# Performance work log

Measured on AMD Instinct MI355X. Metric: run time of the kernel, lower is better.

## Reference

```python
import jax, jax.numpy as jnp
import numpy as np

N = 4096
IN_FEATS = 64
HIDDEN = 128
STEPS = 3
SCALE = 3.0
LJ_EPS = 0.1
LJ_SIGMA = 3.5
LJ_MIX = 0.1  # 'auto' branch: pot = exp(-r/scale)*relu(score) + 0.1*lj
LN_EPS = 1e-5


def setup_inputs() -> dict:
    key = jax.random.key(0)
    ks = jax.random.split(key, 12)
    x = jax.random.normal(ks[0], (N, IN_FEATS), dtype=jnp.float32)
    # sparse-ish 0/1 adjacency (float, as multiplied in the torch code)
    adj = (jax.random.uniform(ks[1], (N, N)) < 0.02).astype(jnp.float32)
    # positive pairwise distances in Angstrom-like range
    dist_mat = jax.random.uniform(ks[2], (N, N), dtype=jnp.float32) * 10.0 + 0.5
    s_in = 1.0 / np.sqrt(IN_FEATS)
    s_h = 1.0 / np.sqrt(HIDDEN)
    s_2h = 1.0 / np.sqrt(2 * HIDDEN)
    params = {
        'W_in': jax.random.uniform(ks[3], (IN_FEATS, HIDDEN), minval=-s_in, maxval=s_in),
        'b_in': jnp.zeros((HIDDEN,), jnp.float32),
        'W_msg': jax.random.uniform(ks[4], (HIDDEN, HIDDEN), minval=-s_h, maxval=s_h),
        'b_msg': jnp.zeros((HIDDEN,), jnp.float32),
        'W_u1': jax.random.uniform(ks[5], (2 * HIDDEN, HIDDEN), minval=-s_2h, maxval=s_2h),
        'b_u1': jnp.zeros((HIDDEN,), jnp.float32),
        'W_u2': jax.random.uniform(ks[6], (HIDDEN, HIDDEN), minval=-s_h, maxval=s_h),
        'b_u2': jnp.zeros((HIDDEN,), jnp.float32),
        'gamma': jnp.ones((HIDDEN,), jnp.float32),
        'beta': jnp.zeros((HIDDEN,), jnp.float32),
    }
    return {'x': x, 'adj': adj, 'dist_mat': dist_mat, **params}


def _layernorm(x, gamma, beta):
    mu = jnp.mean(x, axis=-1, keepdims=True)
    var = jnp.mean(jnp.square(x - mu), axis=-1, keepdims=True)
    return (x - mu) * jax.lax.rsqrt(var + LN_EPS) * gamma + beta


def reference(x, adj, dist_mat, W_in, b_in, W_msg, b_msg, W_u1, b_u1, W_u2, b_u2, gamma, beta):
    h = x @ W_in + b_in  # (n, hidden)
    # distance-only terms are loop-invariant
    r_safe = jnp.clip(dist_mat, 1e-6, None)
    sr6 = (LJ_SIGMA / r_safe) ** 6
    lj = 4.0 * LJ_EPS * (sr6 * sr6 - sr6)          # (n, n)
    decay = jnp.exp(-dist_mat / SCALE)             # (n, n)
    pot_const = LJ_MIX * lj                        # 'auto' branch constant part
    for _ in range(STEPS):
        # torch code computes msg_lin(h) but never uses it (dead code) -> skipped
        # pot_scalar[i,j] = <h_i, h_j>, computed without (n,n,d) materialization
        pot_scalar = h @ h.T                       # (n, n)
        pot = decay * jax.nn.relu(pot_scalar) + pot_const
        # m_i = sum_j pot[i,j]*adj[i,j]*h_j == masked-weighted matmul
        m = (pot * adj) @ h                        # (n, hidden)
        concat = jnp.concatenate([h, m], axis=-1)  # (n, 2*hidden)
        delta = jax.nn.relu(concat @ W_u1 + b_u1) @ W_u2 + b_u2
        h = _layernorm(h + delta, gamma, beta)
    return h
```

## Files before the change

kernel.cpp:

```cpp
#include <hip/hip_runtime.h>
#include <hip/hip_bf16.h>

#define NN   4096
#define HID  128
#define INFE 64
#define KE   160
#define KMAX 192
#define CH   64
#define RPB  4
#define RPB8 8

typedef unsigned short u16;
typedef unsigned int   u32;

__device__ __forceinline__ float bfu(u16 u) { return __uint_as_float(((u32)u) << 16); }
__device__ __forceinline__ float bflo(u32 w){ return __uint_as_float(w << 16); }
__device__ __forceinline__ float bfhi(u32 w){ return __uint_as_float(w & 0xffff0000u); }
__device__ __forceinline__ u16 f2b(float f) { __hip_bfloat16 h = __float2bfloat16(f); return *(u16*)&h; }

template<int CTRL>
__device__ __forceinline__ float dppadd(float v) {
    return v + __uint_as_float((u32)__builtin_amdgcn_update_dpp(
        0, (int)__float_as_uint(v), CTRL, 0xF, 0xF, true));
}

__global__ __launch_bounds__(128) void k_h0(
    const float* __restrict__ x, const float* __restrict__ Win, const float* __restrict__ bin,
    float* __restrict__ hdst, u16* __restrict__ bdst)
{
    __shared__ float xl[INFE];
    const int r = blockIdx.x;
    const int d = threadIdx.x;
    if (d < INFE) xl[d] = x[(size_t)r*INFE + d];
    __syncthreads();
    float acc = bin[d];
    #pragma unroll 8
    for (int k = 0; k < INFE; ++k)
        acc = fmaf(xl[k], Win[k*HID + d], acc);
    hdst[(size_t)r*HID + d] = acc;
    bdst[(size_t)r*HID + d] = f2b(acc);
}

__global__ __launch_bounds__(256) void k_prep(
    const float* __restrict__ adj, const float* __restrict__ dist,
    float4* __restrict__ edges, int* __restrict__ nnzp,
    const float* __restrict__ x, const float* __restrict__ Win, const float* __restrict__ bin,
    float* __restrict__ hdst, u16* __restrict__ bdst)
{
    const int t = threadIdx.x;
    if (blockIdx.x < NN/2) {
        __shared__ int cnt[2];
        __shared__ int   cl[2][KE];
        __shared__ float ca[2][KE];
        const int r0 = blockIdx.x * 2;
        if (t < 2) cnt[t] = 0;
        __syncthreads();
        float4 av[2][4];
        #pragma unroll
        for (int rr = 0; rr < 2; ++rr) {
            const float4* arow = (const float4*)(adj + (size_t)(r0+rr)*NN);
            #pragma unroll
            for (int q = 0; q < 4; ++q) av[rr][q] = arow[t + 256*q];
        }
        #pragma unroll
        for (int rr = 0; rr < 2; ++rr) {
            #pragma unroll
            for (int q = 0; q < 4; ++q) {
                float a4[4] = {av[rr][q].x, av[rr][q].y, av[rr][q].z, av[rr][q].w};
                if (a4[0] != 0.f || a4[1] != 0.f || a4[2] != 0.f || a4[3] != 0.f) {
                    #pragma unroll
                    for (int u = 0; u < 4; ++u) {
                        if (a4[u] != 0.f) {
                            int pos = atomicAdd(&cnt[rr], 1);
                            if (pos < KE) { cl[rr][pos] = 4*(t + 256*q) + u; ca[rr][pos] = a4[u]; }
                        }
                    }
                }
            }
        }
        __syncthreads();
        #pragma unroll
        for (int rr = 0; rr < 2; ++rr) {
            const int n  = cnt[rr] < KE ? cnt[rr] : KE;
            const int np = (n + 31) / 32 * 32;
            float4* erow = edges + (size_t)(r0+rr)*KE;
            for (int i = n + t; i < np; i += 256)
                erow[i] = make_float4(__int_as_float(0), 0.f, 0.f, 0.f);
            const float* drow = dist + (size_t)(r0+rr)*NN;
            for (int i = t; i < n; i += 256) {
                int   c = cl[rr][i];
                float a = ca[rr][i];
                float d  = fmaxf(drow[c], 1e-6f);
                float dw1 = a * __expf(-d * (1.0f/3.0f));
                float tt = 3.5f / d, t2 = tt*tt, t6 = t2*t2*t2;
                float dw2 = a * 0.04f * (t6*t6 - t6);
                erow[i] = make_float4(__int_as_float(c), dw1, dw2, 0.f);
            }
            if (t == 0) nnzp[r0+rr] = np;
        }
    } else {
        __shared__ float xl[2][INFE];
        const int grp = t >> 7;
        const int d   = t & 127;
        const int r   = (blockIdx.x - NN/2) * 2 + grp;
        if (d < INFE) xl[grp][d] = x[(size_t)r*INFE + d];
        __syncthreads();
        float acc = bin[d];
        #pragma unroll 8
        for (int k = 0; k < INFE; ++k)
            acc = fmaf(xl[grp][k], Win[k*HID + d], acc);
        hdst[(size_t)r*HID + d] = acc;
        bdst[(size_t)r*HID + d] = f2b(acc);
    }
}

__global__ __launch_bounds__(512, 4) void k_fstep8(
    const float4* __restrict__ edges, const int* __restrict__ nnzp,
    const float* __restrict__ h, const u16* __restrict__ hb,
    const float* __restrict__ Wu1, const float* __restrict__ bu1,
    const float* __restrict__ Wu2, const float* __restrict__ bu2,
    const float* __restrict__ gam, const float* __restrict__ bet,
    float* __restrict__ hout, u16* __restrict__ bout)
{
    __shared__ __align__(16) float ps[8][RPB8][HID];
    __shared__ __align__(16) float hs[RPB8][HID];
    __shared__ __align__(16) float ms[RPB8][HID];
    __shared__ __align__(16) float h1s[RPB8][HID];
    __shared__ float hn[RPB8][HID];
    const int t    = threadIdx.x;
    const int w    = t >> 6;
    const int lane = t & 63;
    const int ig   = lane & 15;
    const int grp  = lane >> 4;
    const int r0   = blockIdx.x * RPB8;
    const int r    = r0 + w;

    const int np = nnzp[r];
    const float4 hiA = *(const float4*)(h + (size_t)r*HID + 8*ig);
    const float4 hiB = *(const float4*)(h + (size_t)r*HID + 8*ig + 4);
    if (grp == 0) {
        *(float4*)&hs[w][8*ig]     = hiA;
        *(float4*)&hs[w][8*ig + 4] = hiB;
    }

    const float4* erow = edges + (size_t)r*KE;
    float macc[8];
    #pragma unroll
    for (int d = 0; d < 8; ++d) macc[d] = 0.f;
    for (int e0 = 0; e0 < np; e0 += 32) {
        float4 ed[8]; uint4 hj4[8]; float p[8];
        #pragma unroll
        for (int q = 0; q < 8; ++q) ed[q] = erow[e0 + grp + 4*q];
        #pragma unroll
        for (int q = 0; q < 8; ++q) {
            int c = __float_as_int(ed[q].x);
            hj4[q] = *(const uint4*)(hb + (size_t)c*HID + 8*ig);
        }
        #pragma unroll
        for (int q = 0; q < 8; ++q) {
            float j0 = bflo(hj4[q].x), j1 = bfhi(hj4[q].x);
            float j2 = bflo(hj4[q].y), j3 = bfhi(hj4[q].y);
            float j4 = bflo(hj4[q].z), j5 = bfhi(hj4[q].z);
            float j6 = bflo(hj4[q].w), j7 = bfhi(hj4[q].w);
            float pp = hiA.x*j0;
            pp = fmaf(hiA.y, j1, pp); pp = fmaf(hiA.z, j2, pp); pp = fmaf(hiA.w, j3, pp);
            pp = fmaf(hiB.x, j4, pp); pp = fmaf(hiB.y, j5, pp); pp = fmaf(hiB.z, j6, pp);
            p[q] = fmaf(hiB.w, j7, pp);
        }
        #pragma unroll
        for (int q = 0; q < 8; ++q) {
            p[q] = dppadd<0x128>(p[q]);
            p[q] = dppadd<0x124>(p[q]);
            p[q] = dppadd<0x122>(p[q]);
            p[q] = dppadd<0x121>(p[q]);
        }
        #pragma unroll
        for (int q = 0; q < 8; ++q) {
            float wq = fmaf(ed[q].y, fmaxf(p[q], 0.f), ed[q].z);
            float j0 = bflo(hj4[q].x), j1 = bfhi(hj4[q].x);
            float j2 = bflo(hj4[q].y), j3 = bfhi(hj4[q].y);
            float j4 = bflo(hj4[q].z), j5 = bfhi(hj4[q].z);
            float j6 = bflo(hj4[q].w), j7 = bfhi(hj4[q].w);
            macc[0] = fmaf(wq, j0, macc[0]); macc[1] = fmaf(wq, j1, macc[1]);
            macc[2] = fmaf(wq, j2, macc[2]); macc[3] = fmaf(wq, j3, macc[3]);
            macc[4] = fmaf(wq, j4, macc[4]); macc[5] = fmaf(wq, j5, macc[5]);
            macc[6] = fmaf(wq, j6, macc[6]); macc[7] = fmaf(wq, j7, macc[7]);
        }
    }
    #pragma unroll
    for (int d = 0; d < 8; ++d) {
        macc[d] += __shfl_xor(macc[d], 16);
        macc[d] += __shfl_xor(macc[d], 32);
    }
    if (grp == 0) {
        *(float4*)&ms[w][8*ig]     = make_float4(macc[0], macc[1], macc[2], macc[3]);
        *(float4*)&ms[w][8*ig + 4] = make_float4(macc[4], macc[5], macc[6], macc[7]);
    }
    __syncthreads();

    {
        const int kq = t >> 6;
        const int dd = t & 63;
        const float bi0 = (kq == 0) ? bu1[dd]      : 0.f;
        const float bi1 = (kq == 0) ? bu1[dd + 64] : 0.f;
        float a0[RPB8], a1[RPB8];
        #pragma unroll
        for (int rr = 0; rr < RPB8; ++rr) { a0[rr] = bi0; a1[rr] = bi1; }
        const float (*src)[HID] = (kq < 4) ? hs : ms;
        const int kb = (kq & 3) * 32;
        const float* wp = Wu1 + (size_t)(kq * 32) * HID + dd;
        #pragma unroll 2
        for (int k = 0; k < 32; k += 4) {
            float w00 = wp[(k+0)*HID], w01 = wp[(k+0)*HID + 64];
            float w10 = wp[(k+1)*HID], w11 = wp[(k+1)*HID + 64];
            float w20 = wp[(k+2)*HID], w21 = wp[(k+2)*HID + 64];
            float w30 = wp[(k+3)*HID], w31 = wp[(k+3)*HID + 64];
            #pragma unroll
            for (int rr = 0; rr < RPB8; ++rr) {
                float4 c4 = *(const float4*)&src[rr][kb + k];
                a0[rr] = fmaf(c4.x, w00, a0[rr]); a0[rr] = fmaf(c4.y, w10, a0[rr]);
                a0[rr] = fmaf(c4.z, w20, a0[rr]); a0[rr] = fmaf(c4.w, w30, a0[rr]);
                a1[rr] = fmaf(c4.x, w01, a1[rr]); a1[rr] = fmaf(c4.y, w11, a1[rr]);
                a1[rr] = fmaf(c4.z, w21, a1[rr]); a1[rr] = fmaf(c4.w, w31, a1[rr]);
            }
        }
        #pragma unroll
        for (int rr = 0; rr < RPB8; ++rr) {
            ps[kq][rr][dd]      = a0[rr];
            ps[kq][rr][dd + 64] = a1[rr];
        }
    }
    __syncthreads();
    for (int pidx = t; pidx < RPB8*HID; pidx += 512) {
        int rr = pidx >> 7, d = pidx & 127;
        float s = ps[0][rr][d] + ps[1][rr][d] + ps[2][rr][d] + ps[3][rr][d]
                + ps[4][rr][d] + ps[5][rr][d] + ps[6][rr][d] + ps[7][rr][d];
        h1s[rr][d] = fmaxf(s, 0.f);
    }
    __syncthreads();
    {
        const int kq = t >> 6;
        const int dd = t & 63;
        const float bi0 = (kq == 0) ? bu2[dd]      : 0.f;
        const float bi1 = (kq == 0) ? bu2[dd + 64] : 0.f;
        float a0[RPB8], a1[RPB8];
        #pragma unroll
        for (int rr = 0; rr < RPB8; ++rr) { a0[rr] = bi0; a1[rr] = bi1; }
        const int kb = kq * 16;
        const float* wp = Wu2 + (size_t)(kq * 16) * HID + dd;
        #pragma unroll
        for (int k = 0; k < 16; k += 4) {
            float w00 = wp[(k+0)*HID], w01 = wp[(k+0)*HID + 64];
            float w10 = wp[(k+1)*HID], w11 = wp[(k+1)*HID + 64];
            float w20 = wp[(k+2)*HID], w21 = wp[(k+2)*HID + 64];
            float w30 = wp[(k+3)*HID], w31 = wp[(k+3)*HID + 64];
            #pragma unroll
            for (int rr = 0; rr < RPB8; ++rr) {
                float4 c4 = *(const float4*)&h1s[rr][kb + k];
                a0[rr] = fmaf(c4.x, w00, a0[rr]); a0[rr] = fmaf(c4.y, w10, a0[rr]);
                a0[rr] = fmaf(c4.z, w20, a0[rr]); a0[rr] = fmaf(c4.w, w30, a0[rr]);
                a1[rr] = fmaf(c4.x, w01, a1[rr]); a1[rr] = fmaf(c4.y, w11, a1[rr]);
                a1[rr] = fmaf(c4.z, w21, a1[rr]); a1[rr] = fmaf(c4.w, w31, a1[rr]);
            }
        }
        #pragma unroll
        for (int rr = 0; rr < RPB8; ++rr) {
            ps[kq][rr][dd]      = a0[rr];
            ps[kq][rr][dd + 64] = a1[rr];
        }
    }
    __syncthreads();
    for (int pidx = t; pidx < RPB8*HID; pidx += 512) {
        int rr = pidx >> 7, d = pidx & 127;
        hn[rr][d] = hs[rr][d]
                  + ps[0][rr][d] + ps[1][rr][d] + ps[2][rr][d] + ps[3][rr][d]
                  + ps[4][rr][d] + ps[5][rr][d] + ps[6][rr][d] + ps[7][rr][d];
    }
    __syncthreads();
    {
        float v0 = hn[w][lane], v1 = hn[w][lane + 64];
        float s = v0 + v1;
        #pragma unroll
        for (int mask = 1; mask <= 32; mask <<= 1) s += __shfl_xor(s, mask);
        float mu = s * (1.0f/128.0f);
        float z0 = v0 - mu, z1 = v1 - mu;
        float vv = fmaf(z0, z0, z1*z1);
        #pragma unroll
        for (int mask = 1; mask <= 32; mask <<= 1) vv += __shfl_xor(vv, mask);
        float rstd = rsqrtf(vv * (1.0f/128.0f) + 1e-5f);
        float o0 = fmaf(z0 * rstd, gam[lane],      bet[lane]);
        float o1 = fmaf(z1 * rstd, gam[lane + 64], bet[lane + 64]);
        hout[(size_t)r*HID + lane]      = o0;
        hout[(size_t)r*HID + lane + 64] = o1;
        bout[(size_t)r*HID + lane]      = f2b(o0);
        bout[(size_t)r*HID + lane + 64] = f2b(o1);
    }
}

template<bool SB, bool DB>
__global__ __launch_bounds__(128) void k_step(
    const float* __restrict__ adj, const float* __restrict__ dist,
    const void* hsrc, void* hdst,
    const float* __restrict__ Wu1, const float* __restrict__ bu1,
    const float* __restrict__ Wu2, const float* __restrict__ bu2,
    const float* __restrict__ gam, const float* __restrict__ bet)
{
    __shared__ int   cnt4[RPB];
    __shared__ int   cl[RPB][KMAX];
    __shared__ float w1l[RPB][KMAX], w2l[RPB][KMAX];
    __shared__ __align__(16) float hs4[RPB][HID];
    __shared__ __align__(16) float hj[CH][HID + 1];
    __shared__ float pl[CH];
    __shared__ __align__(16) float ms[RPB][HID];
    __shared__ __align__(16) float h1s[RPB][HID];
    __shared__ float hn[RPB][HID];
    const int r0 = blockIdx.x * RPB;
    const int t  = threadIdx.x;
    const u16*   s16 = (const u16*)hsrc;
    const float* s32 = (const float*)hsrc;
    if (t < RPB) cnt4[t] = 0;
    for (int i = t; i < RPB*HID; i += 128) {
        int rr = i >> 7, d = i & 127;
        hs4[rr][d] = SB ? bfu(s16[(size_t)(r0+rr)*HID + d]) : s32[(size_t)(r0+rr)*HID + d];
    }
    __syncthreads();
    for (int idx = t; idx < RPB*(NN/4); idx += 128) {
        int rr = idx >> 10, c4 = idx & 1023;
        float4 a4 = ((const float4*)(adj + (size_t)(r0+rr)*NN))[c4];
        if (a4.x != 0.f || a4.y != 0.f || a4.z != 0.f || a4.w != 0.f) {
            const float* drow = dist + (size_t)(r0+rr)*NN;
            float av4[4] = {a4.x, a4.y, a4.z, a4.w};
            #pragma unroll
            for (int q = 0; q < 4; ++q) {
                float av = av4[q];
                if (av != 0.f) {
                    int c = 4*c4 + q;
                    float d  = fmaxf(drow[c], 1e-6f);
                    float dw1 = av * __expf(-d * (1.0f/3.0f));
                    float tt = 3.5f / d, t2 = tt*tt, t6 = t2*t2*t2;
                    float dw2 = av * 0.04f * (t6*t6 - t6);
                    int pos = atomicAdd(&cnt4[rr], 1);
                    if (pos < KMAX) { cl[rr][pos] = c; w1l[rr][pos] = dw1; w2l[rr][pos] = dw2; }
                }
            }
        }
    }
    __syncthreads();
    int npv[RPB];
    for (int rr = 0; rr < RPB; ++rr) {
        int n  = cnt4[rr] < KMAX ? cnt4[rr] : KMAX;
        int np = (n + CH - 1) / CH * CH;
        npv[rr] = np;
        for (int i = n + t; i < np; i += 128) { cl[rr][i] = 0; w1l[rr][i] = 0.f; w2l[rr][i] = 0.f; }
    }
    __syncthreads();
    const int e2 = t >> 1, hf = t & 1;
    for (int rr = 0; rr < RPB; ++rr) {
        float acc = 0.f;
        for (int e0 = 0; e0 < npv[rr]; e0 += CH) {
            int c = cl[rr][e0 + e2];
            float* dst = &hj[e2][hf*64];
            if (SB) {
                const uint4* sv = (const uint4*)(s16 + (size_t)c*HID + hf*64);
                #pragma unroll
                for (int i = 0; i < 8; ++i) {
                    uint4 v = sv[i];
                    dst[8*i+0] = __uint_as_float(v.x << 16); dst[8*i+1] = __uint_as_float(v.x & 0xffff0000u);
                    dst[8*i+2] = __uint_as_float(v.y << 16); dst[8*i+3] = __uint_as_float(v.y & 0xffff0000u);
                    dst[8*i+4] = __uint_as_float(v.z << 16); dst[8*i+5] = __uint_as_float(v.z & 0xffff0000u);
                    dst[8*i+6] = __uint_as_float(v.w << 16); dst[8*i+7] = __uint_as_float(v.w & 0xffff0000u);
                }
            } else {
                const float4* sv = (const float4*)(s32 + (size_t)c*HID + hf*64);
                #pragma unroll
                for (int i = 0; i < 16; ++i) {
                    float4 v = sv[i];
                    dst[4*i+0] = v.x; dst[4*i+1] = v.y; dst[4*i+2] = v.z; dst[4*i+3] = v.w;
                }
            }
            __syncthreads();
            {
                const float* ha = &hs4[rr][hf*64];
                const float* hb = &hj[e2][hf*64];
                float p = 0.f;
                #pragma unroll
                for (int i = 0; i < 64; ++i) p = fmaf(ha[i], hb[i], p);
                p += __shfl_xor(p, 1);
                if (hf == 0) pl[e2] = fmaf(w1l[rr][e0+e2], fmaxf(p, 0.f), w2l[rr][e0+e2]);
            }
            __syncthreads();
            #pragma unroll
            for (int i = 0; i < CH; ++i) acc = fmaf(pl[i], hj[i][t], acc);
            __syncthreads();
        }
        ms[rr][t] = acc;
    }
    __syncthreads();
    {
        float bb = bu1[t];
        float a0 = bb, a1 = bb, a2 = bb, a3 = bb;
        for (int k = 0; k < HID; k += 4) {
            float w0 = Wu1[(k+0)*HID + t], w1 = Wu1[(k+1)*HID + t];
            float w2 = Wu1[(k+2)*HID + t], w3 = Wu1[(k+3)*HID + t];
            float4 c0 = *(const float4*)&hs4[0][k];
            float4 c1 = *(const float4*)&hs4[1][k];
            float4 c2 = *(const float4*)&hs4[2][k];
            float4 c3 = *(const float4*)&hs4[3][k];
            a0 = fmaf(c0.x,w0,a0); a0 = fmaf(c0.y,w1,a0); a0 = fmaf(c0.z,w2,a0); a0 = fmaf(c0.w,w3,a0);
            a1 = fmaf(c1.x,w0,a1); a1 = fmaf(c1.y,w1,a1); a1 = fmaf(c1.z,w2,a1); a1 = fmaf(c1.w,w3,a1);
            a2 = fmaf(c2.x,w0,a2); a2 = fmaf(c2.y,w1,a2); a2 = fmaf(c2.z,w2,a2); a2 = fmaf(c2.w,w3,a2);
            a3 = fmaf(c3.x,w0,a3); a3 = fmaf(c3.y,w1,a3); a3 = fmaf(c3.z,w2,a3); a3 = fmaf(c3.w,w3,a3);
        }
        for (int k = 0; k < HID; k += 4) {
            float w0 = Wu1[(HID+k+0)*HID + t], w1 = Wu1[(HID+k+1)*HID + t];
            float w2 = Wu1[(HID+k+2)*HID + t], w3 = Wu1[(HID+k+3)*HID + t];
            float4 c0 = *(const float4*)&ms[0][k];
            float4 c1 = *(const float4*)&ms[1][k];
            float4 c2 = *(const float4*)&ms[2][k];
            float4 c3 = *(const float4*)&ms[3][k];
            a0 = fmaf(c0.x,w0,a0); a0 = fmaf(c0.y,w1,a0); a0 = fmaf(c0.z,w2,a0); a0 = fmaf(c0.w,w3,a0);
            a1 = fmaf(c1.x,w0,a1); a1 = fmaf(c1.y,w1,a1); a1 = fmaf(c1.z,w2,a1); a1 = fmaf(c1.w,w3,a1);
            a2 = fmaf(c2.x,w0,a2); a2 = fmaf(c2.y,w1,a2); a2 = fmaf(c2.z,w2,a2); a2 = fmaf(c2.w,w3,a2);
            a3 = fmaf(c3.x,w0,a3); a3 = fmaf(c3.y,w1,a3); a3 = fmaf(c3.z,w2,a3); a3 = fmaf(c3.w,w3,a3);
        }
        h1s[0][t] = fmaxf(a0,0.f); h1s[1][t] = fmaxf(a1,0.f);
        h1s[2][t] = fmaxf(a2,0.f); h1s[3][t] = fmaxf(a3,0.f);
    }
    __syncthreads();
    {
        float bb = bu2[t];
        float b0 = bb, b1 = bb, b2 = bb, b3 = bb;
        for (int k = 0; k < HID; k += 4) {
            float w0 = Wu2[(k+0)*HID + t], w1 = Wu2[(k+1)*HID + t];
            float w2 = Wu2[(k+2)*HID + t], w3 = Wu2[(k+3)*HID + t];
            float4 c0 = *(const float4*)&h1s[0][k];
            float4 c1 = *(const float4*)&h1s[1][k];
            float4 c2 = *(const float4*)&h1s[2][k];
            float4 c3 = *(const float4*)&h1s[3][k];
            b0 = fmaf(c0.x,w0,b0); b0 = fmaf(c0.y,w1,b0); b0 = fmaf(c0.z,w2,b0); b0 = fmaf(c0.w,w3,b0);
            b1 = fmaf(c1.x,w0,b1); b1 = fmaf(c1.y,w1,b1); b1 = fmaf(c1.z,w2,b1); b1 = fmaf(c1.w,w3,b1);
            b2 = fmaf(c2.x,w0,b2); b2 = fmaf(c2.y,w1,b2); b2 = fmaf(c2.z,w2,b2); b2 = fmaf(c2.w,w3,b2);
            b3 = fmaf(c3.x,w0,b3); b3 = fmaf(c3.y,w1,b3); b3 = fmaf(c3.z,w2,b3); b3 = fmaf(c3.w,w3,b3);
        }
        hn[0][t] = hs4[0][t] + b0; hn[1][t] = hs4[1][t] + b1;
        hn[2][t] = hs4[2][t] + b2; hn[3][t] = hs4[3][t] + b3;
    }
    __syncthreads();
    {
        const int lr = t >> 5, j = t & 31;
        float s = 0.f;
        #pragma unroll
        for (int q = 0; q < 4; ++q) s += hn[lr][j + 32*q];
        #pragma unroll
        for (int k2 = 16; k2 >= 1; k2 >>= 1) s += __shfl_xor(s, k2);
        float mu = s * (1.0f/128.0f);
        float v = 0.f;
        #pragma unroll
        for (int q = 0; q < 4; ++q) { float z = hn[lr][j + 32*q] - mu; v = fmaf(z, z, v); }
        #pragma unroll
        for (int k2 = 16; k2 >= 1; k2 >>= 1) v += __shfl_xor(v, k2);
        float rstd = rsqrtf(v * (1.0f/128.0f) + 1e-5f);
        #pragma unroll
        for (int q = 0; q < 4; ++q) {
            int dd = j + 32*q;
            float val = fmaf((hn[lr][dd] - mu) * rstd, gam[dd], bet[dd]);
            if (DB) ((u16*)hdst)[(size_t)(r0+lr)*HID + dd] = f2b(val);
            else    ((float*)hdst)[(size_t)(r0+lr)*HID + dd] = val;
        }
    }
}

extern "C" void kernel_launch(void* const* d_in, const int* in_sizes, int n_in,
                              void* d_out, int out_size, void* d_ws, size_t ws_size,
                              hipStream_t stream)
{
    const float* x    = (const float*)d_in[0];
    const float* adj  = (const float*)d_in[1];
    const float* dist = (const float*)d_in[2];
    const float* Win  = (const float*)d_in[3];
    const float* bin  = (const float*)d_in[4];
    const float* Wu1  = (const float*)d_in[7];
    const float* bu1  = (const float*)d_in[8];
    const float* Wu2  = (const float*)d_in[9];
    const float* bu2  = (const float*)d_in[10];
    const float* gam  = (const float*)d_in[11];
    const float* bet  = (const float*)d_in[12];

    const size_t ebytes = (size_t)NN * KE * sizeof(float4);
    const size_t cbytes = ((size_t)NN * sizeof(int) + 255) & ~255;
    const size_t hb32   = (size_t)NN * HID * sizeof(float);
    const size_t hb16   = (size_t)NN * HID * sizeof(u16);
    const size_t need   = ebytes + cbytes + hb32 + 2*hb16;

    if (ws_size >= need) {
        char* p = (char*)d_ws;
        float4* edges = (float4*)p;            p += ebytes;
        int*    nnzp  = (int*)p;               p += cbytes;
        float*  hA    = (float*)p;             p += hb32;
        u16*    bA    = (u16*)p;               p += hb16;
        u16*    bB    = (u16*)p;               p += hb16;
        float*  hB    = (float*)d_out;

        k_prep<<<NN/2 + NN/2, 256, 0, stream>>>(adj, dist, edges, nnzp, x, Win, bin, hA, bA);
        k_fstep8<<<NN/RPB8, 512, 0, stream>>>(edges, nnzp, hA, bA, Wu1, bu1, Wu2, bu2, gam, bet, hB, bB);
        k_fstep8<<<NN/RPB8, 512, 0, stream>>>(edges, nnzp, hB, bB, Wu1, bu1, Wu2, bu2, gam, bet, hA, bA);
        k_fstep8<<<NN/RPB8, 512, 0, stream>>>(edges, nnzp, hA, bA, Wu1, bu1, Wu2, bu2, gam, bet, hB, bB);
    } else if (ws_size >= hb32) {
        void* A = d_ws; void* B = d_out;
        k_h0<<<NN, 128, 0, stream>>>(x, Win, bin, (float*)A, (u16*)B);
        k_step<false,false><<<NN/RPB, 128, 0, stream>>>(adj, dist, A, B, Wu1, bu1, Wu2, bu2, gam, bet);
        k_step<false,false><<<NN/RPB, 128, 0, stream>>>(adj, dist, B, A, Wu1, bu1, Wu2, bu2, gam, bet);
        k_step<false,false><<<NN/RPB, 128, 0, stream>>>(adj, dist, A, B, Wu1, bu1, Wu2, bu2, gam, bet);
    }
}
```

Before: 224.8 us.

## Fuse prep and three GNN steps into one cooperative persistent kernel

Replaces the four separate launches (edge compaction plus input projection, then three step kernels) with a single cooperative kernel that uses grid-wide syncs between phases. Each block handles 8 rows for prep and reuses the shared-memory pool for the edge lists and the partial sums. The goal is to remove inter-kernel launch gaps and tail drain. It needs all 512 blocks of 512 threads to be co-resident; if the cooperative launch fails, it falls back to the old kernels. Grid syncs add their own barrier cost, and prep now runs fewer, larger blocks.

```diff
diff --git a/kernel.cpp b/kernel.cpp
--- a/kernel.cpp
+++ b/kernel.cpp
@@ -1,5 +1,8 @@
 #include <hip/hip_runtime.h>
 #include <hip/hip_bf16.h>
+#include <hip/hip_cooperative_groups.h>
+
+namespace cg = cooperative_groups;
 
 #define NN   4096
 #define HID  128
@@ -24,126 +27,24 @@
         0, (int)__float_as_uint(v), CTRL, 0xF, 0xF, true));
 }
 
-__global__ __launch_bounds__(128) void k_h0(
-    const float* __restrict__ x, const float* __restrict__ Win, const float* __restrict__ bin,
-    float* __restrict__ hdst, u16* __restrict__ bdst)
-{
-    __shared__ float xl[INFE];
-    const int r = blockIdx.x;
-    const int d = threadIdx.x;
-    if (d < INFE) xl[d] = x[(size_t)r*INFE + d];
-    __syncthreads();
-    float acc = bin[d];
-    #pragma unroll 8
-    for (int k = 0; k < INFE; ++k)
-        acc = fmaf(xl[k], Win[k*HID + d], acc);
-    hdst[(size_t)r*HID + d] = acc;
-    bdst[(size_t)r*HID + d] = f2b(acc);
-}
-
-__global__ __launch_bounds__(256) void k_prep(
-    const float* __restrict__ adj, const float* __restrict__ dist,
-    float4* __restrict__ edges, int* __restrict__ nnzp,
-    const float* __restrict__ x, const float* __restrict__ Win, const float* __restrict__ bin,
-    float* __restrict__ hdst, u16* __restrict__ bdst)
-{
-    const int t = threadIdx.x;
-    if (blockIdx.x < NN/2) {
-        __shared__ int cnt[2];
-        __shared__ int   cl[2][KE];
-        __shared__ float ca[2][KE];
-        const int r0 = blockIdx.x * 2;
-        if (t < 2) cnt[t] = 0;
-        __syncthreads();
-        float4 av[2][4];
-        #pragma unroll
-        for (int rr = 0; rr < 2; ++rr) {
-            const float4* arow = (const float4*)(adj + (size_t)(r0+rr)*NN);
-            #pragma unroll
-            for (int q = 0; q < 4; ++q) av[rr][q] = arow[t + 256*q];
-        }
-        #pragma unroll
-        for (int rr = 0; rr < 2; ++rr) {
-            #pragma unroll
-            for (int q = 0; q < 4; ++q) {
-                float a4[4] = {av[rr][q].x, av[rr][q].y, av[rr][q].z, av[rr][q].w};
-                if (a4[0] != 0.f || a4[1] != 0.f || a4[2] != 0.f || a4[3] != 0.f) {
-                    #pragma unroll
-                    for (int u = 0; u < 4; ++u) {
-                        if (a4[u] != 0.f) {
-                            int pos = atomicAdd(&cnt[rr], 1);
-                            if (pos < KE) { cl[rr][pos] = 4*(t + 256*q) + u; ca[rr][pos] = a4[u]; }
-                        }
-                    }
-                }
-            }
-        }
-        __syncthreads();
-        #pragma unroll
-        for (int rr = 0; rr < 2; ++rr) {
-            const int n  = cnt[rr] < KE ? cnt[rr] : KE;
-            const int np = (n + 31) / 32 * 32;
-            float4* erow = edges + (size_t)(r0+rr)*KE;
-            for (int i = n + t; i < np; i += 256)
-                erow[i] = make_float4(__int_as_float(0), 0.f, 0.f, 0.f);
-            const float* drow = dist + (size_t)(r0+rr)*NN;
-            for (int i = t; i < n; i += 256) {
-                int   c = cl[rr][i];
-                float a = ca[rr][i];
-                float d  = fmaxf(drow[c], 1e-6f);
-                float dw1 = a * __expf(-d * (1.0f/3.0f));
-                float tt = 3.5f / d, t2 = tt*tt, t6 = t2*t2*t2;
-                float dw2 = a * 0.04f * (t6*t6 - t6);
-                erow[i] = make_float4(__int_as_float(c), dw1, dw2, 0.f);
-            }
-            if (t == 0) nnzp[r0+rr] = np;
-        }
-    } else {
-        __shared__ float xl[2][INFE];
-        const int grp = t >> 7;
-        const int d   = t & 127;
-        const int r   = (blockIdx.x - NN/2) * 2 + grp;
-        if (d < INFE) xl[grp][d] = x[(size_t)r*INFE + d];
-        __syncthreads();
-        float acc = bin[d];
-        #pragma unroll 8
-        for (int k = 0; k < INFE; ++k)
-            acc = fmaf(xl[grp][k], Win[k*HID + d], acc);
-        hdst[(size_t)r*HID + d] = acc;
-        bdst[(size_t)r*HID + d] = f2b(acc);
-    }
-}
-
-__global__ __launch_bounds__(512, 4) void k_fstep8(
-    const float4* __restrict__ edges, const int* __restrict__ nnzp,
-    const float* __restrict__ h, const u16* __restrict__ hb,
+__device__ __forceinline__ void gnn_step(
+    int t, int w, int lane, int ig, int grp, int r,
+    const float4* __restrict__ erow, int np,
+    const float* __restrict__ hsrc, const u16* __restrict__ bsrc,
+    float* __restrict__ hdst, u16* __restrict__ bdst,
     const float* __restrict__ Wu1, const float* __restrict__ bu1,
     const float* __restrict__ Wu2, const float* __restrict__ bu2,
     const float* __restrict__ gam, const float* __restrict__ bet,
-    float* __restrict__ hout, u16* __restrict__ bout)
+    float (*ps)[RPB8][HID], float (*hs)[HID], float (*ms)[HID],
+    float (*h1s)[HID], float (*hn)[HID])
 {
-    __shared__ __align__(16) float ps[8][RPB8][HID];
-    __shared__ __align__(16) float hs[RPB8][HID];
-    __shared__ __align__(16) float ms[RPB8][HID];
-    __shared__ __align__(16) float h1s[RPB8][HID];
-    __shared__ float hn[RPB8][HID];
-    const int t    = threadIdx.x;
-    const int w    = t >> 6;
-    const int lane = t & 63;
-    const int ig   = lane & 15;
-    const int grp  = lane >> 4;
-    const int r0   = blockIdx.x * RPB8;
-    const int r    = r0 + w;
-
-    const int np = nnzp[r];
-    const float4 hiA = *(const float4*)(h + (size_t)r*HID + 8*ig);
-    const float4 hiB = *(const float4*)(h + (size_t)r*HID + 8*ig + 4);
+    const float4 hiA = *(const float4*)(hsrc + (size_t)r*HID + 8*ig);
+    const float4 hiB = *(const float4*)(hsrc + (size_t)r*HID + 8*ig + 4);
     if (grp == 0) {
         *(float4*)&hs[w][8*ig]     = hiA;
         *(float4*)&hs[w][8*ig + 4] = hiB;
     }
 
-    const float4* erow = edges + (size_t)r*KE;
     float macc[8];
     #pragma unroll
     for (int d = 0; d < 8; ++d) macc[d] = 0.f;
@@ -154,7 +55,7 @@
         #pragma unroll
         for (int q = 0; q < 8; ++q) {
             int c = __float_as_int(ed[q].x);
-            hj4[q] = *(const uint4*)(hb + (size_t)c*HID + 8*ig);
+            hj4[q] = *(const uint4*)(bsrc + (size_t)c*HID + 8*ig);
         }
         #pragma unroll
         for (int q = 0; q < 8; ++q) {
@@ -290,11 +191,251 @@
         float rstd = rsqrtf(vv * (1.0f/128.0f) + 1e-5f);
         float o0 = fmaf(z0 * rstd, gam[lane],      bet[lane]);
         float o1 = fmaf(z1 * rstd, gam[lane + 64], bet[lane + 64]);
-        hout[(size_t)r*HID + lane]      = o0;
-        hout[(size_t)r*HID + lane + 64] = o1;
-        bout[(size_t)r*HID + lane]      = f2b(o0);
-        bout[(size_t)r*HID + lane + 64] = f2b(o1);
-    }
+        hdst[(size_t)r*HID + lane]      = o0;
+        hdst[(size_t)r*HID + lane + 64] = o1;
+        bdst[(size_t)r*HID + lane]      = f2b(o0);
+        bdst[(size_t)r*HID + lane + 64] = f2b(o1);
+    }
+}
+
+__global__ __launch_bounds__(512, 4) void k_fused(
+    const float* __restrict__ adj, const float* __restrict__ dist,
+    float4* __restrict__ edges,
+    const float* __restrict__ x, const float* __restrict__ Win, const float* __restrict__ bin,
+    float* __restrict__ hA, u16* __restrict__ bA,
+    float* __restrict__ hB, u16* __restrict__ bB,
+    const float* __restrict__ Wu1, const float* __restrict__ bu1,
+    const float* __restrict__ Wu2, const float* __restrict__ bu2,
+    const float* __restrict__ gam, const float* __restrict__ bet)
+{
+    __shared__ __align__(16) char POOL[RPB8*RPB8*HID*4];
+    __shared__ __align__(16) float hs[RPB8][HID];
+    __shared__ __align__(16) float ms[RPB8][HID];
+    __shared__ __align__(16) float h1s[RPB8][HID];
+    __shared__ float hn[RPB8][HID];
+    __shared__ int npl[RPB8];
+    __shared__ int cnt[RPB8];
+    float (*ps)[RPB8][HID] = reinterpret_cast<float(*)[RPB8][HID]>(POOL);
+    int   (*cl)[KE]        = reinterpret_cast<int(*)[KE]>(POOL);
+    float (*ca)[KE]        = reinterpret_cast<float(*)[KE]>(POOL + RPB8*KE*sizeof(int));
+
+    cg::grid_group grid = cg::this_grid();
+    const int t    = threadIdx.x;
+    const int w    = t >> 6;
+    const int lane = t & 63;
+    const int ig   = lane & 15;
+    const int grp  = lane >> 4;
+    const int r0   = blockIdx.x * RPB8;
+    const int r    = r0 + w;
+
+    if (t < RPB8) cnt[t] = 0;
+    float4 av[4][2];
+    #pragma unroll
+    for (int j = 0; j < 4; ++j) {
+        const float4* arow = (const float4*)(adj + (size_t)(r0+j)*NN);
+        av[j][0] = arow[t]; av[j][1] = arow[t + 512];
+    }
+    {
+        float xv = x[(size_t)r*INFE + lane];
+        float acc0 = bin[lane], acc1 = bin[lane + 64];
+        for (int k = 0; k < INFE; ++k) {
+            float xk = __shfl(xv, k);
+            acc0 = fmaf(xk, Win[k*HID + lane],      acc0);
+            acc1 = fmaf(xk, Win[k*HID + lane + 64], acc1);
+        }
+        hA[(size_t)r*HID + lane]      = acc0;
+        hA[(size_t)r*HID + lane + 64] = acc1;
+        bA[(size_t)r*HID + lane]      = f2b(acc0);
+        bA[(size_t)r*HID + lane + 64] = f2b(acc1);
+    }
+    __syncthreads();
+    #pragma unroll
+    for (int j = 0; j < 4; ++j) {
+        #pragma unroll
+        for (int q = 0; q < 2; ++q) {
+            float a4[4] = {av[j][q].x, av[j][q].y, av[j][q].z, av[j][q].w};
+            if (a4[0] != 0.f || a4[1] != 0.f || a4[2] != 0.f || a4[3] != 0.f) {
+                #pragma unroll
+                for (int u = 0; u < 4; ++u) {
+                    if (a4[u] != 0.f) {
+                        int pos = atomicAdd(&cnt[j], 1);
+                        if (pos < KE) { cl[j][pos] = 4*(t + 512*q) + u; ca[j][pos] = a4[u]; }
+                    }
+                }
+            }
+        }
+    }
+    #pragma unroll
+    for (int j = 0; j < 4; ++j) {
+        const float4* arow = (const float4*)(adj + (size_t)(r0+4+j)*NN);
+        av[j][0] = arow[t]; av[j][1] = arow[t + 512];
+    }
+    #pragma unroll
+    for (int j = 0; j < 4; ++j) {
+        #pragma unroll
+        for (int q = 0; q < 2; ++q) {
+            float a4[4] = {av[j][q].x, av[j][q].y, av[j][q].z, av[j][q].w};
+            if (a4[0] != 0.f || a4[1] != 0.f || a4[2] != 0.f || a4[3] != 0.f) {
+                #pragma unroll
+                for (int u = 0; u < 4; ++u) {
+                    if (a4[u] != 0.f) {
+                        int pos = atomicAdd(&cnt[4+j], 1);
+                        if (pos < KE) { cl[4+j][pos] = 4*(t + 512*q) + u; ca[4+j][pos] = a4[u]; }
+                    }
+                }
+            }
+        }
+    }
+    __syncthreads();
+    {
+        int n  = cnt[w] < KE ? cnt[w] : KE;
+        int np = (n + 31) / 32 * 32;
+        float4* erow = edges + (size_t)r*KE;
+        const float* drow = dist + (size_t)r*NN;
+        for (int i = lane; i < n; i += 64) {
+            int   c = cl[w][i];
+            float a = ca[w][i];
+            float d  = fmaxf(drow[c], 1e-6f);
+            float dw1 = a * __expf(-d * (1.0f/3.0f));
+            float tt = 3.5f / d, t2 = tt*tt, t6 = t2*t2*t2;
+            float dw2 = a * 0.04f * (t6*t6 - t6);
+            erow[i] = make_float4(__int_as_float(c), dw1, dw2, 0.f);
+        }
+        for (int i = n + lane; i < np; i += 64)
+            erow[i] = make_float4(__int_as_float(0), 0.f, 0.f, 0.f);
+        if (lane == 0) npl[w] = np;
+    }
+    __threadfence();
+    grid.sync();
+
+    const float4* erow = edges + (size_t)r*KE;
+    const int np = npl[w];
+    gnn_step(t, w, lane, ig, grp, r, erow, np, hA, bA, hB, bB,
+             Wu1, bu1, Wu2, bu2, gam, bet, ps, hs, ms, h1s, hn);
+    __threadfence();
+    grid.sync();
+    gnn_step(t, w, lane, ig, grp, r, erow, np, hB, bB, hA, bA,
+             Wu1, bu1, Wu2, bu2, gam, bet, ps, hs, ms, h1s, hn);
+    __threadfence();
+    grid.sync();
+    gnn_step(t, w, lane, ig, grp, r, erow, np, hA, bA, hB, bB,
+             Wu1, bu1, Wu2, bu2, gam, bet, ps, hs, ms, h1s, hn);
+}
+
+__global__ __launch_bounds__(128) void k_h0(
+    const float* __restrict__ x, const float* __restrict__ Win, const float* __restrict__ bin,
+    float* __restrict__ hdst, u16* __restrict__ bdst)
+{
+    __shared__ float xl[INFE];
+    const int r = blockIdx.x;
+    const int d = threadIdx.x;
+    if (d < INFE) xl[d] = x[(size_t)r*INFE + d];
+    __syncthreads();
+    float acc = bin[d];
+    #pragma unroll 8
+    for (int k = 0; k < INFE; ++k)
+        acc = fmaf(xl[k], Win[k*HID + d], acc);
+    hdst[(size_t)r*HID + d] = acc;
+    bdst[(size_t)r*HID + d] = f2b(acc);
+}
+
+__global__ __launch_bounds__(256) void k_prep(
+    const float* __restrict__ adj, const float* __restrict__ dist,
+    float4* __restrict__ edges, int* __restrict__ nnzp,
+    const float* __restrict__ x, const float* __restrict__ Win, const float* __restrict__ bin,
+    float* __restrict__ hdst, u16* __restrict__ bdst)
+{
+    const int t = threadIdx.x;
+    if (blockIdx.x < NN/2) {
+        __shared__ int cnt[2];
+        __shared__ int   cl[2][KE];
+        __shared__ float ca[2][KE];
+        const int r0 = blockIdx.x * 2;
+        if (t < 2) cnt[t] = 0;
+        __syncthreads();
+        float4 av[2][4];
+        #pragma unroll
+        for (int rr = 0; rr < 2; ++rr) {
+            const float4* arow = (const float4*)(adj + (size_t)(r0+rr)*NN);
+            #pragma unroll
+            for (int q = 0; q < 4; ++q) av[rr][q] = arow[t + 256*q];
+        }
+        #pragma unroll
+        for (int rr = 0; rr < 2; ++rr) {
+            #pragma unroll
+            for (int q = 0; q < 4; ++q) {
+                float a4[4] = {av[rr][q].x, av[rr][q].y, av[rr][q].z, av[rr][q].w};
+                if (a4[0] != 0.f || a4[1] != 0.f || a4[2] != 0.f || a4[3] != 0.f) {
+                    #pragma unroll
+                    for (int u = 0; u < 4; ++u) {
+                        if (a4[u] != 0.f) {
+                            int pos = atomicAdd(&cnt[rr], 1);
+                            if (pos < KE) { cl[rr][pos] = 4*(t + 256*q) + u; ca[rr][pos] = a4[u]; }
+                        }
+                    }
+                }
+            }
+        }
+        __syncthreads();
+        #pragma unroll
+        for (int rr = 0; rr < 2; ++rr) {
+            const int n  = cnt[rr] < KE ? cnt[rr] : KE;
+            const int np = (n + 31) / 32 * 32;
+            float4* erow = edges + (size_t)(r0+rr)*KE;
+            for (int i = n + t; i < np; i += 256)
+                erow[i] = make_float4(__int_as_float(0), 0.f, 0.f, 0.f);
+            const float* drow = dist + (size_t)(r0+rr)*NN;
+            for (int i = t; i < n; i += 256) {
+                int   c = cl[rr][i];
+                float a = ca[rr][i];
+                float d  = fmaxf(drow[c], 1e-6f);
+                float dw1 = a * __expf(-d * (1.0f/3.0f));
+                float tt = 3.5f / d, t2 = tt*tt, t6 = t2*t2*t2;
+                float dw2 = a * 0.04f * (t6*t6 - t6);
+                erow[i] = make_float4(__int_as_float(c), dw1, dw2, 0.f);
+            }
+            if (t == 0) nnzp[r0+rr] = np;
+        }
+    } else {
+        __shared__ float xl[2][INFE];
+        const int grp = t >> 7;
+        const int d   = t & 127;
+        const int r   = (blockIdx.x - NN/2) * 2 + grp;
+        if (d < INFE) xl[grp][d] = x[(size_t)r*INFE + d];
+        __syncthreads();
+        float acc = bin[d];
+        #pragma unroll 8
+        for (int k = 0; k < INFE; ++k)
+            acc = fmaf(xl[grp][k], Win[k*HID + d], acc);
+        hdst[(size_t)r*HID + d] = acc;
+        bdst[(size_t)r*HID + d] = f2b(acc);
+    }
+}
+
+__global__ __launch_bounds__(512, 4) void k_fstep8(
+    const float4* __restrict__ edges, const int* __restrict__ nnzp,
+    const float* __restrict__ h, const u16* __restrict__ hb,
+    const float* __restrict__ Wu1, const float* __restrict__ bu1,
+    const float* __restrict__ Wu2, const float* __restrict__ bu2,
+    const float* __restrict__ gam, const float* __restrict__ bet,
+    float* __restrict__ hout, u16* __restrict__ bout)
+{
+    __shared__ __align__(16) float psb[8][RPB8][HID];
+    __shared__ __align__(16) float hs[RPB8][HID];
+    __shared__ __align__(16) float ms[RPB8][HID];
+    __shared__ __align__(16) float h1s[RPB8][HID];
+    __shared__ float hn[RPB8][HID];
+    const int t    = threadIdx.x;
+    const int w    = t >> 6;
+    const int lane = t & 63;
+    const int ig   = lane & 15;
+    const int grp  = lane >> 4;
+    const int r0   = blockIdx.x * RPB8;
+    const int r    = r0 + w;
+    const int np   = nnzp[r];
+    gnn_step(t, w, lane, ig, grp, r, edges + (size_t)r*KE, np, h, hb, hout, bout,
+             Wu1, bu1, Wu2, bu2, gam, bet,
+             reinterpret_cast<float(*)[RPB8][HID]>(&psb[0][0][0]), hs, ms, h1s, hn);
 }
 
 template<bool SB, bool DB>
@@ -501,10 +642,21 @@
         u16*    bB    = (u16*)p;               p += hb16;
         float*  hB    = (float*)d_out;
 
-        k_prep<<<NN/2 + NN/2, 256, 0, stream>>>(adj, dist, edges, nnzp, x, Win, bin, hA, bA);
-        k_fstep8<<<NN/RPB8, 512, 0, stream>>>(edges, nnzp, hA, bA, Wu1, bu1, Wu2, bu2, gam, bet, hB, bB);
-        k_fstep8<<<NN/RPB8, 512, 0, stream>>>(edges, nnzp, hB, bB, Wu1, bu1, Wu2, bu2, gam, bet, hA, bA);
-        k_fstep8<<<NN/RPB8, 512, 0, stream>>>(edges, nnzp, hA, bA, Wu1, bu1, Wu2, bu2, gam, bet, hB, bB);
+        void* kargs[] = { (void*)&adj, (void*)&dist, (void*)&edges,
+                          (void*)&x, (void*)&Win, (void*)&bin,
+                          (void*)&hA, (void*)&bA, (void*)&hB, (void*)&bB,
+                          (void*)&Wu1, (void*)&bu1, (void*)&Wu2, (void*)&bu2,
+                          (void*)&gam, (void*)&bet };
+        hipError_t e = hipLaunchCooperativeKernel((const void*)k_fused,
+                                                  dim3(NN/RPB8), dim3(512),
+                                                  kargs, 0, stream);
+        if (e != hipSuccess) {
+            (void)hipGetLastError();
+            k_prep<<<NN, 256, 0, stream>>>(adj, dist, edges, nnzp, x, Win, bin, hA, bA);
+            k_fstep8<<<NN/RPB8, 512, 0, stream>>>(edges, nnzp, hA, bA, Wu1, bu1, Wu2, bu2, gam, bet, hB, bB);
+            k_fstep8<<<NN/RPB8, 512, 0, stream>>>(edges, nnzp, hB, bB, Wu1, bu1, Wu2, bu2, gam, bet, hA, bA);
+            k_fstep8<<<NN/RPB8, 512, 0, stream>>>(edges, nnzp, hA, bA, Wu1, bu1, Wu2, bu2, gam, bet, hB, bB);
+        }
     } else if (ws_size >= hb32) {
         void* A = d_ws; void* B = d_out;
         k_h0<<<NN, 128, 0, stream>>>(x, Win, bin, (float*)A, (u16*)B);
```

Measured after the change: 731.2 us. 3.25x slower.
